# Kernel tuning notes

Hardware: AMD Instinct MI355X
Metric: run time of the kernel (lower is better)

The kernel has to match this reference:

```python
import jax, jax.numpy as jnp
import numpy as np

B = 131072   # batch
D = 128      # input_dim
H = 512      # hidden_dim
E = 2        # number of tasks/experts (fixed in module)
O = 2        # output dim (fixed in module)


def setup_inputs() -> dict:
    key = jax.random.key(0)
    k0, k1, k2, k3 = jax.random.split(key, 4)
    x = jax.random.normal(k0, (B, D), jnp.float32)
    # kaiming-uniform-ish scale for weights
    w1 = jax.random.normal(k1, (E, H, D), jnp.float32) * (1.0 / np.sqrt(D).astype(np.float32))
    b1 = jnp.zeros((E, H), jnp.float32)
    w2 = jax.random.normal(k2, (E, O, H), jnp.float32) * (1.0 / np.sqrt(H).astype(np.float32))
    b2 = jnp.zeros((E, O), jnp.float32)
    # buffer is zeros in torch; randomize so routing is non-degenerate
    prototypes = jax.random.normal(k3, (E, D), jnp.float32)
    return {"x": x, "w1": w1, "b1": b1, "w2": w2, "b2": b2, "prototypes": prototypes}


def reference(x, w1, b1, w2, b2, prototypes):
    # Routing: torch.cdist -> argmin. Squared distance has the same argmin
    # as euclidean distance (sqrt is monotone), so skip the sqrt.
    diff = x[:, None, :] - prototypes[None, :, :]          # [B, E, D]
    d2 = jnp.sum(diff * diff, axis=-1)                     # [B, E]
    t = jnp.argmin(d2, axis=1)                             # [B] int

    # Only E=2 experts: evaluate both and select, instead of a per-sample
    # gathered [B,H,D] weight tensor (this replaces the torch python loop).
    h = jax.nn.relu(jnp.einsum('bd,ehd->beh', x, w1) + b1[None])   # [B, E, H]
    out_all = jnp.einsum('beh,eoh->beo', h, w2) + b2[None]          # [B, E, O]
    out = jnp.take_along_axis(out_all, t[:, None, None], axis=1)[:, 0, :]  # [B, O]
    return out
```

## Files before the change

kernel.cpp:

```cpp
#include <hip/hip_runtime.h>

typedef __bf16 bf16x8 __attribute__((ext_vector_type(8)));
typedef float floatx4 __attribute__((ext_vector_type(4)));

#define XS 136

__device__ __forceinline__ unsigned short f32_bf16(float f) {
    union { float f; unsigned int u; } c; c.f = f;
    return (unsigned short)((c.u + 0x7fffu + ((c.u >> 16) & 1u)) >> 16);
}

__global__ __launch_bounds__(256) void prep_w1_frag(const float* __restrict__ w1,
                                                    unsigned short* __restrict__ wbf) {
    int g    = blockIdx.x * 256 + threadIdx.x;
    int lane = g & 63;
    int frag = g >> 6;
    int ks   = frag & 3;
    int nt   = (frag >> 2) & 31;
    int e    = frag >> 7;
    int l15  = lane & 15;
    int quad = lane >> 4;
    int h    = l15 * 32 + nt;
    const float* src = w1 + ((e * 512 + h) * 128 + ks * 32 + quad * 8);
    unsigned short* dst = wbf + (long)g * 8;
    #pragma unroll
    for (int j = 0; j < 8; ++j) dst[j] = f32_bf16(src[j]);
}

__global__ __launch_bounds__(256, 2) void moe_fused(
    const float* __restrict__ x,
    const unsigned short* __restrict__ wbf,
    const float* __restrict__ b1,
    const float* __restrict__ w2,
    const float* __restrict__ b2,
    const float* __restrict__ protos,
    float* __restrict__ out)
{
    __shared__ unsigned short xs[128 * XS];
    __shared__ float out_s[2][128][2][2];
    __shared__ int   t_s[128];

    const int tid   = threadIdx.x;
    const int lane  = tid & 63;
    const int wave  = tid >> 6;
    const int quad  = lane >> 4;
    const int l15   = lane & 15;
    const int slice = wave & 1;
    const int e     = wave >> 1;
    const long rowbase = (long)blockIdx.x * 128;

    {
        int r   = tid >> 1;
        int sub = tid & 1;
        const float* xr = x + (rowbase + r) * 128 + sub * 64;
        const float* p0 = protos + sub * 64;
        const float* p1 = protos + 128 + sub * 64;
        double acc = 0.0;
        #pragma unroll
        for (int k = 0; k < 16; ++k) {
            float4 xv = *(const float4*)(xr + k * 4);
            float4 a  = *(const float4*)(p0 + k * 4);
            float4 b  = *(const float4*)(p1 + k * 4);
            acc += ((double)a.x - b.x) * (0.5 * ((double)a.x + b.x) - xv.x);
            acc += ((double)a.y - b.y) * (0.5 * ((double)a.y + b.y) - xv.y);
            acc += ((double)a.z - b.z) * (0.5 * ((double)a.z + b.z) - xv.z);
            acc += ((double)a.w - b.w) * (0.5 * ((double)a.w + b.w) - xv.w);
        }
        acc += __shfl_xor(acc, 1);
        if (sub == 0) t_s[r] = (acc > 0.0) ? 1 : 0;
    }

    for (int i = tid; i < 128 * 32; i += 256) {
        int r  = i >> 5;
        int c4 = (i & 31) * 4;
        float4 v = *(const float4*)(x + (rowbase + r) * 128 + c4);
        ushort4 p;
        p.x = f32_bf16(v.x); p.y = f32_bf16(v.y);
        p.z = f32_bf16(v.z); p.w = f32_bf16(v.w);
        *(ushort4*)&xs[r * XS + c4] = p;
    }
    __syncthreads();

    bf16x8 afrag[8][4];
    #pragma unroll
    for (int mt = 0; mt < 8; ++mt) {
        int r = mt * 16 + l15;
        #pragma unroll
        for (int ks = 0; ks < 4; ++ks)
            afrag[mt][ks] = *(const bf16x8*)&xs[r * XS + ks * 32 + quad * 8];
    }

    float outp[8][4][2] = {};

    const bf16x8* wb8 = (const bf16x8*)wbf + (long)((e * 32 + slice * 16) * 4) * 64 + lane;
    const int    coff = e * 512 + l15 * 32 + slice * 16;
    const float* b1p  = b1 + coff;
    const float* w2ap = w2 + e * 1024 + l15 * 32 + slice * 16;
    const float* w2bp = w2ap + 512;
    for (int nt = 0; nt < 16; ++nt) {
        const bf16x8* wp = wb8 + nt * 256;
        bf16x8 bf0 = wp[0];
        bf16x8 bf1 = wp[64];
        bf16x8 bf2 = wp[128];
        bf16x8 bf3 = wp[192];
        float bb  = b1p[nt];
        float w2a = w2ap[nt];
        float w2b = w2bp[nt];
        #pragma unroll
        for (int mt = 0; mt < 8; ++mt) {
            floatx4 c = {bb, bb, bb, bb};
            c = __builtin_amdgcn_mfma_f32_16x16x32_bf16(afrag[mt][0], bf0, c, 0, 0, 0);
            c = __builtin_amdgcn_mfma_f32_16x16x32_bf16(afrag[mt][1], bf1, c, 0, 0, 0);
            c = __builtin_amdgcn_mfma_f32_16x16x32_bf16(afrag[mt][2], bf2, c, 0, 0, 0);
            c = __builtin_amdgcn_mfma_f32_16x16x32_bf16(afrag[mt][3], bf3, c, 0, 0, 0);
            #pragma unroll
            for (int rg = 0; rg < 4; ++rg) {
                float h = fmaxf(c[rg], 0.0f);
                outp[mt][rg][0] = fmaf(h, w2a, outp[mt][rg][0]);
                outp[mt][rg][1] = fmaf(h, w2b, outp[mt][rg][1]);
            }
        }
    }

    #pragma unroll
    for (int mt = 0; mt < 8; ++mt)
        #pragma unroll
        for (int rg = 0; rg < 4; ++rg) {
            float v0 = outp[mt][rg][0];
            float v1 = outp[mt][rg][1];
            v0 += __shfl_xor(v0, 1);  v1 += __shfl_xor(v1, 1);
            v0 += __shfl_xor(v0, 2);  v1 += __shfl_xor(v1, 2);
            v0 += __shfl_xor(v0, 4);  v1 += __shfl_xor(v1, 4);
            v0 += __shfl_xor(v0, 8);  v1 += __shfl_xor(v1, 8);
            if (l15 == 0) {
                int r = mt * 16 + quad * 4 + rg;
                out_s[slice][r][e][0] = v0;
                out_s[slice][r][e][1] = v1;
            }
        }
    __syncthreads();

    {
        int r  = tid >> 1;
        int o  = tid & 1;
        int te = t_s[r];
        out[(rowbase + r) * 2 + o] =
            out_s[0][r][te][o] + out_s[1][r][te][o] + b2[te * 2 + o];
    }
}

extern "C" void kernel_launch(void* const* d_in, const int* in_sizes, int n_in,
                              void* d_out, int out_size, void* d_ws, size_t ws_size,
                              hipStream_t stream) {
    const float* x      = (const float*)d_in[0];
    const float* w1     = (const float*)d_in[1];
    const float* b1     = (const float*)d_in[2];
    const float* w2     = (const float*)d_in[3];
    const float* b2     = (const float*)d_in[4];
    const float* protos = (const float*)d_in[5];
    float* out = (float*)d_out;
    unsigned short* wbf = (unsigned short*)d_ws;

    prep_w1_frag<<<dim3(64), dim3(256), 0, stream>>>(w1, wbf);
    moe_fused<<<dim3(1024), dim3(256), 0, stream>>>(x, wbf, b1, w2, b2, protos, out);
}
```

Before: 160.3 us.

## Route rows to experts in-block and compute only the selected expert

Rows in each block are partitioned by their routed expert using ballot and popcount to build per-expert permutation lists. The x tile is staged into shared memory grouped by expert, with each group padded to a multiple of 16 rows. Each expert's waves then run MFMA only for the tiles that hold rows assigned to that expert, which roughly halves the matmul work. The cost is extra synchronisation, permutation bookkeeping, and predicated loops that may complicate register allocation. Load balance now depends on the routing split, because within a block the wave pairs for the two experts get uneven work.

```diff
diff --git a/kernel.cpp b/kernel.cpp
--- a/kernel.cpp
+++ b/kernel.cpp
@@ -4,6 +4,8 @@
 typedef float floatx4 __attribute__((ext_vector_type(4)));
 
 #define XS 136
+#define ROWS 128
+#define PADROWS 144
 
 __device__ __forceinline__ unsigned short f32_bf16(float f) {
     union { float f; unsigned int u; } c; c.f = f;
@@ -36,9 +38,11 @@
     const float* __restrict__ protos,
     float* __restrict__ out)
 {
-    __shared__ unsigned short xs[128 * XS];
-    __shared__ float out_s[2][128][2][2];
-    __shared__ int   t_s[128];
+    __shared__ unsigned short xs[PADROWS * XS];
+    __shared__ float out_s[2][ROWS][2];
+    __shared__ int   t_s[ROWS];
+    __shared__ unsigned short perm_s[2][ROWS];
+    __shared__ int   c1w[2];
 
     const int tid   = threadIdx.x;
     const int lane  = tid & 63;
@@ -47,7 +51,7 @@
     const int l15   = lane & 15;
     const int slice = wave & 1;
     const int e     = wave >> 1;
-    const long rowbase = (long)blockIdx.x * 128;
+    const long rowbase = (long)blockIdx.x * ROWS;
 
     {
         int r   = tid >> 1;
@@ -69,25 +73,61 @@
         acc += __shfl_xor(acc, 1);
         if (sub == 0) t_s[r] = (acc > 0.0) ? 1 : 0;
     }
-
-    for (int i = tid; i < 128 * 32; i += 256) {
-        int r  = i >> 5;
+    __syncthreads();
+
+    unsigned long long m1 = 0;
+    int myt = 0;
+    if (tid < 128) {
+        myt = t_s[tid];
+        m1  = __ballot(myt == 1);
+        if ((tid & 63) == 0) c1w[tid >> 6] = __popcll(m1);
+    }
+    __syncthreads();
+    if (tid < 128) {
+        int w  = tid >> 6;
+        int ln = tid & 63;
+        unsigned long long lt = (((unsigned long long)1) << ln) - 1;
+        int below1 = __popcll(m1 & lt);
+        int r1 = (w ? c1w[0] : 0) + below1;
+        int r0 = (w ? 64 - c1w[0] : 0) + (ln - below1);
+        if (myt) perm_s[1][r1] = (unsigned short)tid;
+        else     perm_s[0][r0] = (unsigned short)tid;
+    }
+    __syncthreads();
+
+    const int n1 = c1w[0] + c1w[1];
+    const int n0 = ROWS - n1;
+    const int P  = (n0 + 15) & ~15;
+
+    for (int i = tid; i < PADROWS * 32; i += 256) {
+        int p  = i >> 5;
         int c4 = (i & 31) * 4;
-        float4 v = *(const float4*)(x + (rowbase + r) * 128 + c4);
-        ushort4 p;
-        p.x = f32_bf16(v.x); p.y = f32_bf16(v.y);
-        p.z = f32_bf16(v.z); p.w = f32_bf16(v.w);
-        *(ushort4*)&xs[r * XS + c4] = p;
-    }
-    __syncthreads();
+        ushort4 pk = {0, 0, 0, 0};
+        int src = -1;
+        if (p < n0)                    src = perm_s[0][p];
+        else if (p >= P && p - P < n1) src = perm_s[1][p - P];
+        if (src >= 0) {
+            float4 v = *(const float4*)(x + (rowbase + src) * 128 + c4);
+            pk.x = f32_bf16(v.x); pk.y = f32_bf16(v.y);
+            pk.z = f32_bf16(v.z); pk.w = f32_bf16(v.w);
+        }
+        *(ushort4*)&xs[p * XS + c4] = pk;
+    }
+    __syncthreads();
+
+    const int ne    = e ? n1 : n0;
+    const int Te    = __builtin_amdgcn_readfirstlane((ne + 15) >> 4);
+    const int pbase = e ? P : 0;
 
     bf16x8 afrag[8][4];
     #pragma unroll
     for (int mt = 0; mt < 8; ++mt) {
-        int r = mt * 16 + l15;
-        #pragma unroll
-        for (int ks = 0; ks < 4; ++ks)
-            afrag[mt][ks] = *(const bf16x8*)&xs[r * XS + ks * 32 + quad * 8];
+        if (mt < Te) {
+            int r = pbase + mt * 16 + l15;
+            #pragma unroll
+            for (int ks = 0; ks < 4; ++ks)
+                afrag[mt][ks] = *(const bf16x8*)&xs[r * XS + ks * 32 + quad * 8];
+        }
     }
 
     float outp[8][4][2] = {};
@@ -108,36 +148,44 @@
         float w2b = w2bp[nt];
         #pragma unroll
         for (int mt = 0; mt < 8; ++mt) {
-            floatx4 c = {bb, bb, bb, bb};
-            c = __builtin_amdgcn_mfma_f32_16x16x32_bf16(afrag[mt][0], bf0, c, 0, 0, 0);
-            c = __builtin_amdgcn_mfma_f32_16x16x32_bf16(afrag[mt][1], bf1, c, 0, 0, 0);
-            c = __builtin_amdgcn_mfma_f32_16x16x32_bf16(afrag[mt][2], bf2, c, 0, 0, 0);
-            c = __builtin_amdgcn_mfma_f32_16x16x32_bf16(afrag[mt][3], bf3, c, 0, 0, 0);
+            if (mt < Te) {
+                floatx4 c = {bb, bb, bb, bb};
+                c = __builtin_amdgcn_mfma_f32_16x16x32_bf16(afrag[mt][0], bf0, c, 0, 0, 0);
+                c = __builtin_amdgcn_mfma_f32_16x16x32_bf16(afrag[mt][1], bf1, c, 0, 0, 0);
+                c = __builtin_amdgcn_mfma_f32_16x16x32_bf16(afrag[mt][2], bf2, c, 0, 0, 0);
+                c = __builtin_amdgcn_mfma_f32_16x16x32_bf16(afrag[mt][3], bf3, c, 0, 0, 0);
+                #pragma unroll
+                for (int rg = 0; rg < 4; ++rg) {
+                    float h = fmaxf(c[rg], 0.0f);
+                    outp[mt][rg][0] = fmaf(h, w2a, outp[mt][rg][0]);
+                    outp[mt][rg][1] = fmaf(h, w2b, outp[mt][rg][1]);
+                }
+            }
+        }
+    }
+
+    #pragma unroll
+    for (int mt = 0; mt < 8; ++mt) {
+        if (mt < Te) {
             #pragma unroll
             for (int rg = 0; rg < 4; ++rg) {
-                float h = fmaxf(c[rg], 0.0f);
-                outp[mt][rg][0] = fmaf(h, w2a, outp[mt][rg][0]);
-                outp[mt][rg][1] = fmaf(h, w2b, outp[mt][rg][1]);
+                float v0 = outp[mt][rg][0];
+                float v1 = outp[mt][rg][1];
+                v0 += __shfl_xor(v0, 1);  v1 += __shfl_xor(v1, 1);
+                v0 += __shfl_xor(v0, 2);  v1 += __shfl_xor(v1, 2);
+                v0 += __shfl_xor(v0, 4);  v1 += __shfl_xor(v1, 4);
+                v0 += __shfl_xor(v0, 8);  v1 += __shfl_xor(v1, 8);
+                if (l15 == 0) {
+                    int p = mt * 16 + quad * 4 + rg;
+                    if (p < ne) {
+                        int r = perm_s[e][p];
+                        out_s[slice][r][0] = v0;
+                        out_s[slice][r][1] = v1;
+                    }
+                }
             }
         }
     }
-
-    #pragma unroll
-    for (int mt = 0; mt < 8; ++mt)
-        #pragma unroll
-        for (int rg = 0; rg < 4; ++rg) {
-            float v0 = outp[mt][rg][0];
-            float v1 = outp[mt][rg][1];
-            v0 += __shfl_xor(v0, 1);  v1 += __shfl_xor(v1, 1);
-            v0 += __shfl_xor(v0, 2);  v1 += __shfl_xor(v1, 2);
-            v0 += __shfl_xor(v0, 4);  v1 += __shfl_xor(v1, 4);
-            v0 += __shfl_xor(v0, 8);  v1 += __shfl_xor(v1, 8);
-            if (l15 == 0) {
-                int r = mt * 16 + quad * 4 + rg;
-                out_s[slice][r][e][0] = v0;
-                out_s[slice][r][e][1] = v1;
-            }
-        }
     __syncthreads();
 
     {
@@ -145,7 +193,7 @@
         int o  = tid & 1;
         int te = t_s[r];
         out[(rowbase + r) * 2 + o] =
-            out_s[0][r][te][o] + out_s[1][r][te][o] + b2[te * 2 + o];
+            out_s[0][r][o] + out_s[1][r][o] + b2[te * 2 + o];
     }
 }
 
```

Result: slower. 165.4 us (+3.2%).
